# Kernel optimization log

Measured on AMD Instinct MI355X. Metric: run time of the kernel, lower is better.

Reference implementation:

```python
import jax, jax.numpy as jnp
import numpy as np
from jax import lax

LAMBDA_REG = 0.01


def setup_inputs() -> dict:
    key = jax.random.key(0)
    k1, k2 = jax.random.split(key)
    features = jax.random.normal(k1, (8192, 512), dtype=jnp.float32)
    attention_scores = jax.random.uniform(k2, (8192,), dtype=jnp.float32)
    return {"features": features, "attention_scores": attention_scores, "k": 256}


def _kernel_matrix(features, attention_scores, lambda_reg=LAMBDA_REG):
    # L_ij = sqrt(q_i q_j) * <f_i, f_j>/(|f_i||f_j|) + lambda * I
    fn = features / jnp.linalg.norm(features, axis=1, keepdims=True)
    S = fn @ fn.T                                   # [N, N] cosine similarity
    q = attention_scores
    L = jnp.sqrt(q[:, None] * q[None, :]) * S
    N = features.shape[0]
    return L + lambda_reg * jnp.eye(N, dtype=features.dtype)


def _greedy_map(L, k):
    # Fast greedy DPP MAP (Chen et al. 2018): incremental Cholesky.
    # Marginal log-det gain of adding item i to selected set Y is log d_i,
    # where d_i = L_ii - ||c_i||^2 is the Schur complement. argmax over d_i
    # equals argmax over logdet(L_{Y+i}) since logdet(L_{Y+i}) = logdet(L_Y) + log d_i.
    N = L.shape[0]

    def step(carry, t):
        d, cis, mask = carry                         # d:[N], cis:[k,N], mask:[N]
        j = jnp.argmax(jnp.where(mask, d, -jnp.inf))  # first max (matches torch '>' tie-break)
        # e_n = (L[j,n] - sum_t cis[t,j]*cis[t,n]) / sqrt(d_j); unused rows of cis are zero
        e = (L[j] - cis[:, j] @ cis) / jnp.sqrt(d[j])  # [N]
        cis = cis.at[t].set(e)
        return (d - e * e, cis, mask.at[j].set(False)), j

    init = (jnp.diagonal(L), jnp.zeros((k, N), L.dtype), jnp.ones(N, dtype=bool))
    _, idx = lax.scan(step, init, jnp.arange(k))
    return idx                                        # [k] int selected indices


def reference(features, attention_scores, k):
    L = _kernel_matrix(features, attention_scores)
    return _greedy_map(L, k)
```

## Files before the change

kernel.cpp:

```cpp
#include <hip/hip_runtime.h>
#include <math.h>
#include <stdint.h>


#define N 8192
#define D 512
#define K 256
#define LAMBDA_REG 0.01f
#define NBLK 256
#define NTHR 256
#define ROWS 32
#define RS   560
#define CS   68
#define CTS  264
#define SSTR 8
#define SCOPE __HIP_MEMORY_SCOPE_AGENT

typedef unsigned long long u64;
typedef float f32x4 __attribute__((ext_vector_type(4)));

struct __align__(8) Pick { float v; int i; };

__device__ __forceinline__ bool better(float av, int ai, float bv, int bi) {
    return (av > bv) || (av == bv && ai < bi);
}

__device__ __forceinline__ u64 pack_slot(float v, int idx, int tag) {
    unsigned hi = ((unsigned)tag << 13) | (unsigned)idx;
    return ((u64)hi << 32) | (u64)__float_as_uint(v);
}

__device__ __forceinline__ void bypass_store_u64(u64* p, u64 v) {
    asm volatile("global_store_dwordx2 %0, %1, off sc0 sc1"
                 :: "v"(p), "v"(v) : "memory");
}

__device__ __forceinline__ void bypass_store_f32x4(const f32x4* p, f32x4 v) {
    asm volatile("global_store_dwordx4 %0, %1, off sc0 sc1"
                 :: "v"(p), "v"(v) : "memory");
}

__global__ __launch_bounds__(NTHR, 1) void dpp_kernel(
        const float* __restrict__ F, const float* __restrict__ q,
        float* __restrict__ FN, float* __restrict__ cisT,
        u64* __restrict__ slots, int* __restrict__ out)
{
    const int tid = threadIdx.x;
    const int blk = blockIdx.x;
    const int r   = tid >> 3;
    const int c   = tid & 7;
    const int n   = blk * ROWS + r;

    __shared__ __align__(16) float lds_fn[ROWS * RS];
    __shared__ __align__(16) float lds_ct[ROWS * CTS];
    __shared__ __align__(16) float lds_gj[8 * CS];
    __shared__ __align__(16) float lds_cj[K];
    __shared__ Pick lds_wave[NTHR / 64];
    __shared__ Pick lds_final;

    const f32x4* F4  = reinterpret_cast<const f32x4*>(F);
    f32x4*       FN4 = reinterpret_cast<f32x4*>(FN);

    float dloc, qn;
    bool  masked = false;
    {
        const f32x4* src = F4 + (size_t)n * (D / 4) + c * 16;
        float* frow = &lds_fn[r * RS + c * CS];
        float ss = 0.f;
        #pragma unroll
        for (int i = 0; i < 16; ++i) {
            f32x4 v = src[i];
            *reinterpret_cast<f32x4*>(frow + 4 * i) = v;
            ss = fmaf(v.x, v.x, ss); ss = fmaf(v.y, v.y, ss);
            ss = fmaf(v.z, v.z, ss); ss = fmaf(v.w, v.w, ss);
        }
        ss += __shfl_xor(ss, 1); ss += __shfl_xor(ss, 2); ss += __shfl_xor(ss, 4);
        const float norm = sqrtf(ss);
        f32x4* dst = FN4 + (size_t)n * (D / 4) + c * 16;
        float ssn = 0.f;
        #pragma unroll
        for (int i = 0; i < 16; ++i) {
            f32x4 v = *reinterpret_cast<f32x4*>(frow + 4 * i);
            v.x /= norm; v.y /= norm; v.z /= norm; v.w /= norm;
            *reinterpret_cast<f32x4*>(frow + 4 * i) = v;
            bypass_store_f32x4(dst + i, v);
            ssn = fmaf(v.x, v.x, ssn); ssn = fmaf(v.y, v.y, ssn);
            ssn = fmaf(v.z, v.z, ssn); ssn = fmaf(v.w, v.w, ssn);
        }
        ssn += __shfl_xor(ssn, 1); ssn += __shfl_xor(ssn, 2); ssn += __shfl_xor(ssn, 4);
        qn = q[n];
        dloc = fmaf(sqrtf(qn * qn), ssn, LAMBDA_REG);
    }

    {
        float v = dloc; int idx = n;
        #pragma unroll
        for (int m = 32; m > 0; m >>= 1) {
            float ov = __shfl_xor(v, m);
            int   oi = __shfl_xor(idx, m);
            if (better(ov, oi, v, idx)) { v = ov; idx = oi; }
        }
        if ((tid & 63) == 0) { lds_wave[tid >> 6].v = v; lds_wave[tid >> 6].i = idx; }
        asm volatile("s_waitcnt vmcnt(0)" ::: "memory");
        __syncthreads();
        if (tid == 0) {
            Pick p = lds_wave[0];
            #pragma unroll
            for (int w = 1; w < NTHR / 64; ++w) {
                Pick o = lds_wave[w];
                if (better(o.v, o.i, p.v, p.i)) p = o;
            }
            bypass_store_u64(&slots[blk * SSTR], pack_slot(p.v, p.i, 0));
        }
    }

    for (int t = 0; t < K; ++t) {
        const unsigned want = (unsigned)t;

        if (tid < 64) {
            const u64* pb = slots + (t & 1) * NBLK * SSTR;
            u64 x0, x1, x2, x3;
            while (true) {
                x0 = __hip_atomic_load(pb + (tid * 4 + 0) * SSTR, __ATOMIC_RELAXED, SCOPE);
                x1 = __hip_atomic_load(pb + (tid * 4 + 1) * SSTR, __ATOMIC_RELAXED, SCOPE);
                x2 = __hip_atomic_load(pb + (tid * 4 + 2) * SSTR, __ATOMIC_RELAXED, SCOPE);
                x3 = __hip_atomic_load(pb + (tid * 4 + 3) * SSTR, __ATOMIC_RELAXED, SCOPE);
                bool ok = ((unsigned)(x0 >> 45) == want) &&
                          ((unsigned)(x1 >> 45) == want) &&
                          ((unsigned)(x2 >> 45) == want) &&
                          ((unsigned)(x3 >> 45) == want);
                if (__all(ok)) break;
                __builtin_amdgcn_s_sleep(1);
            }
            asm volatile("" ::: "memory");
            float v = __uint_as_float((unsigned)x0);
            int idx = (int)((x0 >> 32) & 8191u);
            {
                float w = __uint_as_float((unsigned)x1); int k1 = (int)((x1 >> 32) & 8191u);
                if (better(w, k1, v, idx)) { v = w; idx = k1; }
                w = __uint_as_float((unsigned)x2); k1 = (int)((x2 >> 32) & 8191u);
                if (better(w, k1, v, idx)) { v = w; idx = k1; }
                w = __uint_as_float((unsigned)x3); k1 = (int)((x3 >> 32) & 8191u);
                if (better(w, k1, v, idx)) { v = w; idx = k1; }
            }
            #pragma unroll
            for (int m = 32; m > 0; m >>= 1) {
                float ov = __shfl_xor(v, m);
                int   oi = __shfl_xor(idx, m);
                if (better(ov, oi, v, idx)) { v = ov; idx = oi; }
            }
            if (tid == 0) { lds_final.v = v; lds_final.i = idx; }
        }
        __syncthreads();
        const float dj = lds_final.v;
        const int   j  = lds_final.i;

        if (blk == 0 && tid == 0) out[t] = j;
        if (t == K - 1) break;

        const float sj = sqrtf(dj);
        const float qj = q[j];

        f32x4 gv;
        float cv0, cv1;
        int   tt0 = tid - 128, tt1 = tid;
        if (tid < 128) {
            gv = FN4[(size_t)j * (D / 4) + tid];
        } else {
            if (tt0 < t) cv0 = cisT[(size_t)j * K + tt0];
            if (tt1 < t) cv1 = cisT[(size_t)j * K + tt1];
        }
        if (tid < 128) {
            *reinterpret_cast<f32x4*>(&lds_gj[(tid >> 4) * CS + (tid & 15) * 4]) = gv;
        } else {
            if (tt0 < t) lds_cj[tt0] = cv0;
            if (tt1 < t) lds_cj[tt1] = cv1;
        }
        __syncthreads();

        const float* frow = &lds_fn[r * RS + c * CS];
        const float* grow = &lds_gj[c * CS];
        f32x4 a = {0.f, 0.f, 0.f, 0.f};
        #pragma unroll
        for (int i = 0; i < 16; ++i) {
            f32x4 v = *reinterpret_cast<const f32x4*>(frow + 4 * i);
            f32x4 g = *reinterpret_cast<const f32x4*>(grow + 4 * i);
            a.x = fmaf(v.x, g.x, a.x); a.y = fmaf(v.y, g.y, a.y);
            a.z = fmaf(v.z, g.z, a.z); a.w = fmaf(v.w, g.w, a.w);
        }
        float dot = (a.x + a.y) + (a.z + a.w);
        dot += __shfl_xor(dot, 1); dot += __shfl_xor(dot, 2); dot += __shfl_xor(dot, 4);
        float Ljn = sqrtf(qj * qn) * dot;
        if (n == j) Ljn += LAMBDA_REG;

        float cd = 0.f;
        const float* ctrow = &lds_ct[r * CTS];
        for (int tt = c; tt < t; tt += 8)
            cd = fmaf(lds_cj[tt], ctrow[tt], cd);
        cd += __shfl_xor(cd, 1); cd += __shfl_xor(cd, 2); cd += __shfl_xor(cd, 4);

        const float e = (Ljn - cd) / sj;
        if (c == 0) {
            lds_ct[r * CTS + t] = e;
            const float* ep = cisT + (size_t)n * K + t;
            asm volatile("global_store_dword %0, %1, off sc0 sc1"
                         :: "v"(ep), "v"(e) : "memory");
        }
        dloc = fmaf(-e, e, dloc);
        if (n == j) masked = true;

        {
            float v = masked ? -INFINITY : dloc; int idx = n;
            #pragma unroll
            for (int m = 32; m > 0; m >>= 1) {
                float ov = __shfl_xor(v, m);
                int   oi = __shfl_xor(idx, m);
                if (better(ov, oi, v, idx)) { v = ov; idx = oi; }
            }
            if ((tid & 63) == 0) { lds_wave[tid >> 6].v = v; lds_wave[tid >> 6].i = idx; }
        }
        asm volatile("s_waitcnt vmcnt(0)" ::: "memory");
        __syncthreads();
        if (tid == 0) {
            Pick p = lds_wave[0];
            #pragma unroll
            for (int w = 1; w < NTHR / 64; ++w) {
                Pick o = lds_wave[w];
                if (better(o.v, o.i, p.v, p.i)) p = o;
            }
            bypass_store_u64(&slots[(((t + 1) & 1) * NBLK + blk) * SSTR],
                             pack_slot(p.v, p.i, t + 1));
        }
    }
}

extern "C" void kernel_launch(void* const* d_in, const int* in_sizes, int n_in,
                              void* d_out, int out_size, void* d_ws, size_t ws_size,
                              hipStream_t stream) {
    const float* F = (const float*)d_in[0];
    const float* q = (const float*)d_in[1];
    int* out = (int*)d_out;

    uint8_t* w = (uint8_t*)d_ws;
    u64*   slots = (u64*)(w + 4096);
    float* FN    = (float*)(w + 131072);
    float* cisT  = (float*)(w + 131072 + (size_t)N * D * 4);

    hipMemsetAsync((void*)w, 0xFF, 65536, stream);
    hipLaunchKernelGGL(dpp_kernel, dim3(NBLK), dim3(NTHR), 0, stream,
                       F, q, FN, cisT, slots, out);
}
```

Measured before the change: 1.177 ms.

## Publish per-wave argmax slots and reduce across waves after polling

Each wavefront now writes its own packed argmax slot, 1024 in total, instead of the block combining four waves under a barrier and thread 0 writing one slot. All four waves poll a quarter of the slots each and reduce them, then combine the four results through LDS after the barrier that already existed. This removes one __syncthreads, a serial thread-0 reduction and a vmcnt wait from every one of the 256 greedy steps. The cost is four times as many slots to poll and a larger workspace memset. Dropping the explicit vmcnt wait before publishing may weaken ordering between the cisT store and the slot publish.

Result: slower. 1.710 ms (+45.3%).

```diff
diff --git a/kernel.cpp b/kernel.cpp
--- a/kernel.cpp
+++ b/kernel.cpp
@@ -9,6 +9,7 @@
 #define LAMBDA_REG 0.01f
 #define NBLK 256
 #define NTHR 256
+#define NWAVE 1024
 #define ROWS 32
 #define RS   560
 #define CS   68
@@ -45,18 +46,20 @@
         float* __restrict__ FN, float* __restrict__ cisT,
         u64* __restrict__ slots, int* __restrict__ out)
 {
-    const int tid = threadIdx.x;
-    const int blk = blockIdx.x;
-    const int r   = tid >> 3;
-    const int c   = tid & 7;
-    const int n   = blk * ROWS + r;
+    const int tid  = threadIdx.x;
+    const int blk  = blockIdx.x;
+    const int wid  = tid >> 6;
+    const int lane = tid & 63;
+    const int r    = tid >> 3;
+    const int c    = tid & 7;
+    const int n    = blk * ROWS + r;
+    const int gw   = blk * 4 + wid;
 
     __shared__ __align__(16) float lds_fn[ROWS * RS];
     __shared__ __align__(16) float lds_ct[ROWS * CTS];
     __shared__ __align__(16) float lds_gj[8 * CS];
     __shared__ __align__(16) float lds_cj[K];
-    __shared__ Pick lds_wave[NTHR / 64];
-    __shared__ Pick lds_final;
+    __shared__ Pick lds_wave[4];
 
     const f32x4* F4  = reinterpret_cast<const f32x4*>(F);
     f32x4*       FN4 = reinterpret_cast<f32x4*>(FN);
@@ -100,31 +103,23 @@
             int   oi = __shfl_xor(idx, m);
             if (better(ov, oi, v, idx)) { v = ov; idx = oi; }
         }
-        if ((tid & 63) == 0) { lds_wave[tid >> 6].v = v; lds_wave[tid >> 6].i = idx; }
         asm volatile("s_waitcnt vmcnt(0)" ::: "memory");
-        __syncthreads();
-        if (tid == 0) {
-            Pick p = lds_wave[0];
-            #pragma unroll
-            for (int w = 1; w < NTHR / 64; ++w) {
-                Pick o = lds_wave[w];
-                if (better(o.v, o.i, p.v, p.i)) p = o;
-            }
-            bypass_store_u64(&slots[blk * SSTR], pack_slot(p.v, p.i, 0));
-        }
+        if (lane == 0)
+            bypass_store_u64(&slots[gw * SSTR], pack_slot(v, idx, 0));
     }
 
     for (int t = 0; t < K; ++t) {
         const unsigned want = (unsigned)t;
 
-        if (tid < 64) {
-            const u64* pb = slots + (t & 1) * NBLK * SSTR;
+        {
+            const u64* pb = slots + (t & 1) * NWAVE * SSTR;
+            const int s0 = wid * 256 + lane * 4;
             u64 x0, x1, x2, x3;
             while (true) {
-                x0 = __hip_atomic_load(pb + (tid * 4 + 0) * SSTR, __ATOMIC_RELAXED, SCOPE);
-                x1 = __hip_atomic_load(pb + (tid * 4 + 1) * SSTR, __ATOMIC_RELAXED, SCOPE);
-                x2 = __hip_atomic_load(pb + (tid * 4 + 2) * SSTR, __ATOMIC_RELAXED, SCOPE);
-                x3 = __hip_atomic_load(pb + (tid * 4 + 3) * SSTR, __ATOMIC_RELAXED, SCOPE);
+                x0 = __hip_atomic_load(pb + (s0 + 0) * SSTR, __ATOMIC_RELAXED, SCOPE);
+                x1 = __hip_atomic_load(pb + (s0 + 1) * SSTR, __ATOMIC_RELAXED, SCOPE);
+                x2 = __hip_atomic_load(pb + (s0 + 2) * SSTR, __ATOMIC_RELAXED, SCOPE);
+                x3 = __hip_atomic_load(pb + (s0 + 3) * SSTR, __ATOMIC_RELAXED, SCOPE);
                 bool ok = ((unsigned)(x0 >> 45) == want) &&
                           ((unsigned)(x1 >> 45) == want) &&
                           ((unsigned)(x2 >> 45) == want) &&
@@ -149,11 +144,19 @@
                 int   oi = __shfl_xor(idx, m);
                 if (better(ov, oi, v, idx)) { v = ov; idx = oi; }
             }
-            if (tid == 0) { lds_final.v = v; lds_final.i = idx; }
+            if (lane == 0) { lds_wave[wid].v = v; lds_wave[wid].i = idx; }
         }
         __syncthreads();
-        const float dj = lds_final.v;
-        const int   j  = lds_final.i;
+        float dj; int j;
+        {
+            Pick p = lds_wave[0];
+            #pragma unroll
+            for (int w = 1; w < 4; ++w) {
+                Pick o = lds_wave[w];
+                if (better(o.v, o.i, p.v, p.i)) p = o;
+            }
+            dj = p.v; j = p.i;
+        }
 
         if (blk == 0 && tid == 0) out[t] = j;
         if (t == K - 1) break;
@@ -217,19 +220,9 @@
                 int   oi = __shfl_xor(idx, m);
                 if (better(ov, oi, v, idx)) { v = ov; idx = oi; }
             }
-            if ((tid & 63) == 0) { lds_wave[tid >> 6].v = v; lds_wave[tid >> 6].i = idx; }
-        }
-        asm volatile("s_waitcnt vmcnt(0)" ::: "memory");
-        __syncthreads();
-        if (tid == 0) {
-            Pick p = lds_wave[0];
-            #pragma unroll
-            for (int w = 1; w < NTHR / 64; ++w) {
-                Pick o = lds_wave[w];
-                if (better(o.v, o.i, p.v, p.i)) p = o;
-            }
-            bypass_store_u64(&slots[(((t + 1) & 1) * NBLK + blk) * SSTR],
-                             pack_slot(p.v, p.i, t + 1));
+            if (lane == 0)
+                bypass_store_u64(&slots[(((t + 1) & 1) * NWAVE + gw) * SSTR],
+                                 pack_slot(v, idx, t + 1));
         }
     }
 }
@@ -243,10 +236,10 @@
 
     uint8_t* w = (uint8_t*)d_ws;
     u64*   slots = (u64*)(w + 4096);
-    float* FN    = (float*)(w + 131072);
-    float* cisT  = (float*)(w + 131072 + (size_t)N * D * 4);
-
-    hipMemsetAsync((void*)w, 0xFF, 65536, stream);
+    float* FN    = (float*)(w + 262144);
+    float* cisT  = (float*)(w + 262144 + (size_t)N * D * 4);
+
+    hipMemsetAsync((void*)w, 0xFF, 262144, stream);
     hipLaunchKernelGGL(dpp_kernel, dim3(NBLK), dim3(NTHR), 0, stream,
                        F, q, FN, cisT, slots, out);
 }
```

## Keep normalized feature rows in registers and read selected row from global directly

Applied to the files above, without the earlier changes.

Each thread now holds its normalized 64-float slice of its feature row in sixteen vector registers instead of staging it in shared memory. The selected row g_j is read straight from global memory (L2/L1-resident) inside the dot product, rather than being staged through a shared buffer. The end-of-step wait is relaxed from vmcnt(0) plus syncthreads to an lgkmcnt wait plus a raw s_barrier. This removes shared-memory traffic and one stage of latency per greedy step, at the cost of higher register use. It also risks publishing the slot before other blocks can see the cisT stores.

Measured after the change: 1.557 ms. +32.3%, slower.

```diff
diff --git a/kernel.cpp b/kernel.cpp
--- a/kernel.cpp
+++ b/kernel.cpp
@@ -10,8 +10,6 @@
 #define NBLK 256
 #define NTHR 256
 #define ROWS 32
-#define RS   560
-#define CS   68
 #define CTS  264
 #define SSTR 8
 #define SCOPE __HIP_MEMORY_SCOPE_AGENT
@@ -45,49 +43,64 @@
         float* __restrict__ FN, float* __restrict__ cisT,
         u64* __restrict__ slots, int* __restrict__ out)
 {
-    const int tid = threadIdx.x;
-    const int blk = blockIdx.x;
-    const int r   = tid >> 3;
-    const int c   = tid & 7;
-    const int n   = blk * ROWS + r;
-
-    __shared__ __align__(16) float lds_fn[ROWS * RS];
+    const int tid  = threadIdx.x;
+    const int blk  = blockIdx.x;
+    const int wid  = tid >> 6;
+    const int lane = tid & 63;
+    const int r    = tid >> 3;
+    const int c    = tid & 7;
+    const int n    = blk * ROWS + r;
+
     __shared__ __align__(16) float lds_ct[ROWS * CTS];
-    __shared__ __align__(16) float lds_gj[8 * CS];
     __shared__ __align__(16) float lds_cj[K];
-    __shared__ Pick lds_wave[NTHR / 64];
+    __shared__ Pick lds_wave[4];
     __shared__ Pick lds_final;
 
     const f32x4* F4  = reinterpret_cast<const f32x4*>(F);
     f32x4*       FN4 = reinterpret_cast<f32x4*>(FN);
 
+    f32x4 v00, v01, v02, v03, v04, v05, v06, v07,
+          v08, v09, v10, v11, v12, v13, v14, v15;
     float dloc, qn;
     bool  masked = false;
     {
         const f32x4* src = F4 + (size_t)n * (D / 4) + c * 16;
-        float* frow = &lds_fn[r * RS + c * CS];
+        v00 = src[0];  v01 = src[1];  v02 = src[2];  v03 = src[3];
+        v04 = src[4];  v05 = src[5];  v06 = src[6];  v07 = src[7];
+        v08 = src[8];  v09 = src[9];  v10 = src[10]; v11 = src[11];
+        v12 = src[12]; v13 = src[13]; v14 = src[14]; v15 = src[15];
         float ss = 0.f;
-        #pragma unroll
-        for (int i = 0; i < 16; ++i) {
-            f32x4 v = src[i];
-            *reinterpret_cast<f32x4*>(frow + 4 * i) = v;
-            ss = fmaf(v.x, v.x, ss); ss = fmaf(v.y, v.y, ss);
-            ss = fmaf(v.z, v.z, ss); ss = fmaf(v.w, v.w, ss);
-        }
+#define ACC_SS(vv) ss = fmaf(vv.x, vv.x, ss); ss = fmaf(vv.y, vv.y, ss); \
+                   ss = fmaf(vv.z, vv.z, ss); ss = fmaf(vv.w, vv.w, ss);
+        ACC_SS(v00) ACC_SS(v01) ACC_SS(v02) ACC_SS(v03)
+        ACC_SS(v04) ACC_SS(v05) ACC_SS(v06) ACC_SS(v07)
+        ACC_SS(v08) ACC_SS(v09) ACC_SS(v10) ACC_SS(v11)
+        ACC_SS(v12) ACC_SS(v13) ACC_SS(v14) ACC_SS(v15)
+#undef ACC_SS
         ss += __shfl_xor(ss, 1); ss += __shfl_xor(ss, 2); ss += __shfl_xor(ss, 4);
         const float norm = sqrtf(ss);
+#define NRM(vv) vv.x /= norm; vv.y /= norm; vv.z /= norm; vv.w /= norm;
+        NRM(v00) NRM(v01) NRM(v02) NRM(v03) NRM(v04) NRM(v05) NRM(v06) NRM(v07)
+        NRM(v08) NRM(v09) NRM(v10) NRM(v11) NRM(v12) NRM(v13) NRM(v14) NRM(v15)
+#undef NRM
+        float ssn = 0.f;
+#define ACC_SSN(vv) ssn = fmaf(vv.x, vv.x, ssn); ssn = fmaf(vv.y, vv.y, ssn); \
+                    ssn = fmaf(vv.z, vv.z, ssn); ssn = fmaf(vv.w, vv.w, ssn);
+        ACC_SSN(v00) ACC_SSN(v01) ACC_SSN(v02) ACC_SSN(v03)
+        ACC_SSN(v04) ACC_SSN(v05) ACC_SSN(v06) ACC_SSN(v07)
+        ACC_SSN(v08) ACC_SSN(v09) ACC_SSN(v10) ACC_SSN(v11)
+        ACC_SSN(v12) ACC_SSN(v13) ACC_SSN(v14) ACC_SSN(v15)
+#undef ACC_SSN
+        ssn += __shfl_xor(ssn, 1); ssn += __shfl_xor(ssn, 2); ssn += __shfl_xor(ssn, 4);
         f32x4* dst = FN4 + (size_t)n * (D / 4) + c * 16;
-        float ssn = 0.f;
-        #pragma unroll
-        for (int i = 0; i < 16; ++i) {
-            f32x4 v = *reinterpret_cast<f32x4*>(frow + 4 * i);
-            v.x /= norm; v.y /= norm; v.z /= norm; v.w /= norm;
-            *reinterpret_cast<f32x4*>(frow + 4 * i) = v;
-            bypass_store_f32x4(dst + i, v);
-            ssn = fmaf(v.x, v.x, ssn); ssn = fmaf(v.y, v.y, ssn);
-            ssn = fmaf(v.z, v.z, ssn); ssn = fmaf(v.w, v.w, ssn);
-        }
-        ssn += __shfl_xor(ssn, 1); ssn += __shfl_xor(ssn, 2); ssn += __shfl_xor(ssn, 4);
+        bypass_store_f32x4(dst + 0,  v00); bypass_store_f32x4(dst + 1,  v01);
+        bypass_store_f32x4(dst + 2,  v02); bypass_store_f32x4(dst + 3,  v03);
+        bypass_store_f32x4(dst + 4,  v04); bypass_store_f32x4(dst + 5,  v05);
+        bypass_store_f32x4(dst + 6,  v06); bypass_store_f32x4(dst + 7,  v07);
+        bypass_store_f32x4(dst + 8,  v08); bypass_store_f32x4(dst + 9,  v09);
+        bypass_store_f32x4(dst + 10, v10); bypass_store_f32x4(dst + 11, v11);
+        bypass_store_f32x4(dst + 12, v12); bypass_store_f32x4(dst + 13, v13);
+        bypass_store_f32x4(dst + 14, v14); bypass_store_f32x4(dst + 15, v15);
         qn = q[n];
         dloc = fmaf(sqrtf(qn * qn), ssn, LAMBDA_REG);
     }
@@ -100,13 +113,13 @@
             int   oi = __shfl_xor(idx, m);
             if (better(ov, oi, v, idx)) { v = ov; idx = oi; }
         }
-        if ((tid & 63) == 0) { lds_wave[tid >> 6].v = v; lds_wave[tid >> 6].i = idx; }
+        if (lane == 0) { lds_wave[wid].v = v; lds_wave[wid].i = idx; }
         asm volatile("s_waitcnt vmcnt(0)" ::: "memory");
         __syncthreads();
         if (tid == 0) {
             Pick p = lds_wave[0];
             #pragma unroll
-            for (int w = 1; w < NTHR / 64; ++w) {
+            for (int w = 1; w < 4; ++w) {
                 Pick o = lds_wave[w];
                 if (better(o.v, o.i, p.v, p.i)) p = o;
             }
@@ -161,33 +174,19 @@
         const float sj = sqrtf(dj);
         const float qj = q[j];
 
-        f32x4 gv;
-        float cv0, cv1;
-        int   tt0 = tid - 128, tt1 = tid;
-        if (tid < 128) {
-            gv = FN4[(size_t)j * (D / 4) + tid];
-        } else {
-            if (tt0 < t) cv0 = cisT[(size_t)j * K + tt0];
-            if (tt1 < t) cv1 = cisT[(size_t)j * K + tt1];
-        }
-        if (tid < 128) {
-            *reinterpret_cast<f32x4*>(&lds_gj[(tid >> 4) * CS + (tid & 15) * 4]) = gv;
-        } else {
-            if (tt0 < t) lds_cj[tt0] = cv0;
-            if (tt1 < t) lds_cj[tt1] = cv1;
-        }
+        if (tid < t) lds_cj[tid] = cisT[(size_t)j * K + tid];
         __syncthreads();
 
-        const float* frow = &lds_fn[r * RS + c * CS];
-        const float* grow = &lds_gj[c * CS];
+        const f32x4* gj = FN4 + (size_t)j * (D / 4) + c * 16;
         f32x4 a = {0.f, 0.f, 0.f, 0.f};
-        #pragma unroll
-        for (int i = 0; i < 16; ++i) {
-            f32x4 v = *reinterpret_cast<const f32x4*>(frow + 4 * i);
-            f32x4 g = *reinterpret_cast<const f32x4*>(grow + 4 * i);
-            a.x = fmaf(v.x, g.x, a.x); a.y = fmaf(v.y, g.y, a.y);
-            a.z = fmaf(v.z, g.z, a.z); a.w = fmaf(v.w, g.w, a.w);
-        }
+#define DOT(vv, i) { f32x4 g = gj[i]; \
+        a.x = fmaf(vv.x, g.x, a.x); a.y = fmaf(vv.y, g.y, a.y); \
+        a.z = fmaf(vv.z, g.z, a.z); a.w = fmaf(vv.w, g.w, a.w); }
+        DOT(v00, 0)  DOT(v01, 1)  DOT(v02, 2)  DOT(v03, 3)
+        DOT(v04, 4)  DOT(v05, 5)  DOT(v06, 6)  DOT(v07, 7)
+        DOT(v08, 8)  DOT(v09, 9)  DOT(v10, 10) DOT(v11, 11)
+        DOT(v12, 12) DOT(v13, 13) DOT(v14, 14) DOT(v15, 15)
+#undef DOT
         float dot = (a.x + a.y) + (a.z + a.w);
         dot += __shfl_xor(dot, 1); dot += __shfl_xor(dot, 2); dot += __shfl_xor(dot, 4);
         float Ljn = sqrtf(qj * qn) * dot;
@@ -217,14 +216,16 @@
                 int   oi = __shfl_xor(idx, m);
                 if (better(ov, oi, v, idx)) { v = ov; idx = oi; }
             }
-            if ((tid & 63) == 0) { lds_wave[tid >> 6].v = v; lds_wave[tid >> 6].i = idx; }
-        }
-        asm volatile("s_waitcnt vmcnt(0)" ::: "memory");
-        __syncthreads();
+            if (lane == 0) { lds_wave[wid].v = v; lds_wave[wid].i = idx; }
+        }
+        asm volatile("s_waitcnt lgkmcnt(0)" ::: "memory");
+        __builtin_amdgcn_sched_barrier(0);
+        __builtin_amdgcn_s_barrier();
+        __builtin_amdgcn_sched_barrier(0);
         if (tid == 0) {
             Pick p = lds_wave[0];
             #pragma unroll
-            for (int w = 1; w < NTHR / 64; ++w) {
+            for (int w = 1; w < 4; ++w) {
                 Pick o = lds_wave[w];
                 if (better(o.v, o.i, p.v, p.i)) p = o;
             }
```
